# Optimization experiments

Hardware: AMD Instinct MI355X
Metric: run time of the kernel (lower is better)

Reference implementation:

```python
import jax, jax.numpy as jnp
import numpy as np

B, L, H = 4096, 4096, 1024  # batch, num_labels, hidden_size


def setup_inputs() -> dict:
    key = jax.random.key(0)
    k1, k2, k3, k4, k5 = jax.random.split(key, 5)
    return {
        "bert_output": jax.random.normal(k1, (B, H), dtype=jnp.float32),
        "label_embed": jax.random.normal(k2, (L, H), dtype=jnp.float32),
        "W": jax.random.normal(k3, (L, H), dtype=jnp.float32) * 0.02,
        "b": jax.random.normal(k4, (L,), dtype=jnp.float32) * 0.02,
        "labels": jax.random.randint(k5, (B, L), 0, 2, dtype=jnp.int32),
    }


def reference(bert_output, label_embed, W, b, labels):
    # Original: output[i, j] = classifier(bert_output[i] + label_embed[j])[j]
    #         = sum_k (x[i,k] + E[j,k]) * W[j,k] + b[j]
    #         = (x @ W^T)[i,j] + (E * W).sum(-1)[j] + b[j]
    xWt = jnp.einsum('bh,lh->bl', bert_output, W)          # [B, L] GEMM
    diag_bias = jnp.sum(label_embed * W, axis=-1) + b       # [L] epilogue
    logits = xWt + diag_bias[None, :]                       # [B, L]
    return logits
```

## Files before the change

### kernel.cpp

```cpp
#include <hip/hip_runtime.h>
#include <hip/hip_bf16.h>

#define Bdim 4096
#define Ldim 4096
#define Hdim 1024
#define BM 256
#define BN 256
#define BK 64
#define NT (Hdim / BK)

typedef __attribute__((ext_vector_type(8))) __bf16 bf16x8;
typedef __attribute__((ext_vector_type(4))) float floatx4;

__device__ __forceinline__ unsigned short f2bf(float f) {
  union { __hip_bfloat16 h; unsigned short u; } c;
  c.h = __float2bfloat16(f);
  return c.u;
}

__global__ __launch_bounds__(256) void prep_kernel(
    const float* __restrict__ X, const float* __restrict__ E,
    const float* __restrict__ W, const float* __restrict__ b,
    unsigned short* __restrict__ Xb, unsigned short* __restrict__ Wb,
    float* __restrict__ bias) {
  const int blk = blockIdx.x;
  const int t = threadIdx.x;
  if (blk < 1024) {
    const int wave = t >> 6;
    const int lane = t & 63;
    const int row = blk * 4 + wave;
    const float4* wrow = reinterpret_cast<const float4*>(W + (size_t)row * Hdim);
    const float4* erow = reinterpret_cast<const float4*>(E + (size_t)row * Hdim);
    ushort4* wbrow = reinterpret_cast<ushort4*>(Wb + (size_t)row * Hdim);
    float dot = 0.f;
#pragma unroll
    for (int j = 0; j < 4; ++j) {
      const int idx = lane + j * 64;
      const float4 wv = wrow[idx];
      const float4 ev = erow[idx];
      ushort4 o;
      o.x = f2bf(wv.x); o.y = f2bf(wv.y); o.z = f2bf(wv.z); o.w = f2bf(wv.w);
      wbrow[idx] = o;
      dot += wv.x * ev.x + wv.y * ev.y + wv.z * ev.z + wv.w * ev.w;
    }
#pragma unroll
    for (int off = 32; off > 0; off >>= 1) dot += __shfl_down(dot, off, 64);
    if (lane == 0) bias[row] = dot + b[row];
  } else {
    const int base = (blk - 1024) * 1024 + t;
    const float4* xs = reinterpret_cast<const float4*>(X);
    ushort4* xd = reinterpret_cast<ushort4*>(Xb);
#pragma unroll
    for (int j = 0; j < 4; ++j) {
      const float4 v = xs[base + j * 256];
      ushort4 o;
      o.x = f2bf(v.x); o.y = f2bf(v.y); o.z = f2bf(v.z); o.w = f2bf(v.w);
      xd[base + j * 256] = o;
    }
  }
}

__global__ __launch_bounds__(512, 2) void gemm_bias_kernel(
    const unsigned short* __restrict__ A,
    const unsigned short* __restrict__ Bw,
    const float* __restrict__ bias,
    float* __restrict__ C) {
  __shared__ __align__(16) unsigned short lds[2][2][BM * BK];

  const int tid = threadIdx.x;
  const int wave = tid >> 6;
  const int lane = tid & 63;
  const int wm = wave >> 2;
  const int wn = wave & 3;
  const int m_blk = blockIdx.y * BM;
  const int n_blk = blockIdx.x * BN;

  const int srow = wave * 8 + (lane >> 3);
  const int skofs = ((lane & 7) ^ (lane >> 3)) * 8;
  const unsigned short* gA = A + (size_t)(m_blk + srow) * Hdim + skofs;
  const unsigned short* gB = Bw + (size_t)(n_blk + srow) * Hdim + skofs;

  const int fr = lane & 15;
  const int fq = lane >> 4;
  const int kx0 = ((fq) ^ (fr & 7)) * 8;
  const int kx1 = ((4 + fq) ^ (fr & 7)) * 8;
  const int aBase = (wm * 128 + fr) * BK;
  const int bBase = (wn * 64 + fr) * BK;

  floatx4 acc[8][4] = {};
  bf16x8 af[8][2], bfv[4][2];

#define GLL(src, dst)                                                  \
  __builtin_amdgcn_global_load_lds(                                    \
      (const __attribute__((address_space(1))) void*)(src),            \
      (__attribute__((address_space(3))) void*)(dst), 16, 0, 0)

#define STAGE_H(c, mat, h, kt)                                         \
  do {                                                                 \
    const unsigned short* _g = (mat) ? gB : gA;                        \
    GLL(_g + (size_t)((h) * 128) * Hdim + (size_t)(kt) * BK,           \
        &lds[c][mat][((h) * 128 + wave * 8) * BK]);                    \
    GLL(_g + (size_t)((h) * 128 + 64) * Hdim + (size_t)(kt) * BK,      \
        &lds[c][mat][((h) * 128 + 64 + wave * 8) * BK]);               \
  } while (0)

#define READ_A(c, lo)                                                  \
  do {                                                                 \
    _Pragma("unroll") for (int mi = (lo); mi < (lo) + 4; ++mi) {       \
      af[mi][0] = *(const bf16x8*)&lds[c][0][aBase + mi * 16 * BK + kx0]; \
      af[mi][1] = *(const bf16x8*)&lds[c][0][aBase + mi * 16 * BK + kx1]; \
    }                                                                  \
  } while (0)

#define READ_B(c, lo)                                                  \
  do {                                                                 \
    _Pragma("unroll") for (int ni = (lo); ni < (lo) + 2; ++ni) {       \
      bfv[ni][0] = *(const bf16x8*)&lds[c][1][bBase + ni * 16 * BK + kx0]; \
      bfv[ni][1] = *(const bf16x8*)&lds[c][1][bBase + ni * 16 * BK + kx1]; \
    }                                                                  \
  } while (0)

#define MFMA_Q(M0, N0)                                                 \
  do {                                                                 \
    __builtin_amdgcn_s_setprio(1);                                     \
    _Pragma("unroll") for (int mi = (M0); mi < (M0) + 4; ++mi)         \
      _Pragma("unroll") for (int ni = (N0); ni < (N0) + 2; ++ni) {     \
        acc[mi][ni] = __builtin_amdgcn_mfma_f32_16x16x32_bf16(         \
            af[mi][0], bfv[ni][0], acc[mi][ni], 0, 0, 0);              \
        acc[mi][ni] = __builtin_amdgcn_mfma_f32_16x16x32_bf16(         \
            af[mi][1], bfv[ni][1], acc[mi][ni], 0, 0, 0);              \
      }                                                                \
    __builtin_amdgcn_s_setprio(0);                                     \
  } while (0)

#define BAR __builtin_amdgcn_s_barrier()
#define LGKM0 asm volatile("s_waitcnt lgkmcnt(0)" ::: "memory")
#define GATE4 asm volatile("s_waitcnt vmcnt(4)\n\ts_barrier" ::: "memory")
#define GATE0 asm volatile("s_waitcnt vmcnt(0)\n\ts_barrier" ::: "memory")

#define TILE_BODY(c, o, kt, DO_B, DO_A, GATE)                          \
  do {                                                                 \
                                                               \
    if (DO_B) STAGE_H(o, 1, 0, (kt) + 1);                              \
    READ_A(c, 0);                                                      \
    READ_B(c, 0);                                                      \
    BAR; LGKM0;                                                        \
    MFMA_Q(0, 0);                                                      \
                                                               \
    if (DO_B) STAGE_H(o, 1, 1, (kt) + 1);                              \
    READ_A(c, 4);                                                      \
    BAR; LGKM0;                                                        \
    MFMA_Q(4, 0);                                                      \
    BAR;   \
                                                               \
    if (DO_A) STAGE_H(c, 0, 0, (kt) + 2);                              \
    READ_B(c, 2);                                                      \
    BAR; LGKM0;                                                        \
    MFMA_Q(0, 2);                                                      \
    BAR;                  \
                                                               \
    if (DO_A) STAGE_H(c, 0, 1, (kt) + 2);                              \
    GATE;                                                              \
    MFMA_Q(4, 2);                                                      \
  } while (0)

  STAGE_H(0, 0, 0, 0);
  STAGE_H(0, 0, 1, 0);
  STAGE_H(0, 1, 0, 0);
  STAGE_H(0, 1, 1, 0);
  STAGE_H(1, 0, 0, 1);
  STAGE_H(1, 0, 1, 1);
  GATE4;

#pragma unroll 1
  for (int t = 0; t < NT - 2; t += 2) {
    TILE_BODY(0, 1, t, 1, 1, GATE4);
    TILE_BODY(1, 0, t + 1, 1, 1, GATE4);
  }
  TILE_BODY(0, 1, NT - 2, 1, 0, GATE0);
  TILE_BODY(1, 0, NT - 1, 0, 0, (void)0);

#undef GLL
#undef STAGE_H
#undef READ_A
#undef READ_B
#undef MFMA_Q
#undef BAR
#undef LGKM0
#undef GATE4
#undef GATE0
#undef TILE_BODY

  const int col0 = n_blk + wn * 64 + fr;
  const int row0 = m_blk + wm * 128 + fq * 4;
#pragma unroll
  for (int ni = 0; ni < 4; ++ni) {
    const float bs = bias[col0 + ni * 16];
#pragma unroll
    for (int mi = 0; mi < 8; ++mi) {
      float* cp = C + (size_t)(row0 + mi * 16) * Ldim + (col0 + ni * 16);
      floatx4 v = acc[mi][ni];
      cp[0 * (size_t)Ldim] = v.x + bs;
      cp[1 * (size_t)Ldim] = v.y + bs;
      cp[2 * (size_t)Ldim] = v.z + bs;
      cp[3 * (size_t)Ldim] = v.w + bs;
    }
  }
}

extern "C" void kernel_launch(void* const* d_in, const int* in_sizes, int n_in,
                              void* d_out, int out_size, void* d_ws, size_t ws_size,
                              hipStream_t stream) {
  const float* X = (const float*)d_in[0];
  const float* E = (const float*)d_in[1];
  const float* W = (const float*)d_in[2];
  const float* b = (const float*)d_in[3];
  float* out = (float*)d_out;

  unsigned short* Xb = (unsigned short*)d_ws;
  unsigned short* Wb = Xb + (size_t)Bdim * Hdim;
  float* bias = (float*)(Wb + (size_t)Ldim * Hdim);

  prep_kernel<<<2048, 256, 0, stream>>>(X, E, W, b, Xb, Wb, bias);
  dim3 grid(Ldim / BN, Bdim / BM);
  gemm_bias_kernel<<<grid, 512, 0, stream>>>(Xb, Wb, bias, out);
}
```

Measured before the change: 49.62 us.

## Shrink GEMM tile to 128x256x32 and raise occupancy to four blocks per CU

Halves the M tile and K step, cutting per-wave accumulators from 32 to 16 MFMA tiles. This lowers register and LDS use so launch bounds can request four blocks per SM instead of two. The staging and swizzle are rewritten for the 32-wide K slice, with a one-deep vmcnt gate, and the grid must double along M. The cost is lower arithmetic intensity per LDS byte and twice as many barrier-gated iterations, which raises global and LDS traffic per flop.

```diff
diff --git a/kernel.cpp b/kernel.cpp
--- a/kernel.cpp
+++ b/kernel.cpp
@@ -4,9 +4,9 @@
 #define Bdim 4096
 #define Ldim 4096
 #define Hdim 1024
-#define BM 256
+#define BM 128
 #define BN 256
-#define BK 64
+#define BK 32
 #define NT (Hdim / BK)
 
 typedef __attribute__((ext_vector_type(8))) __bf16 bf16x8;
@@ -60,12 +60,13 @@
   }
 }
 
-__global__ __launch_bounds__(512, 2) void gemm_bias_kernel(
+__global__ __launch_bounds__(512, 4) void gemm_bias_kernel(
     const unsigned short* __restrict__ A,
     const unsigned short* __restrict__ Bw,
     const float* __restrict__ bias,
     float* __restrict__ C) {
-  __shared__ __align__(16) unsigned short lds[2][2][BM * BK];
+  __shared__ __align__(16) unsigned short ldsA[2][BM * BK];
+  __shared__ __align__(16) unsigned short ldsB[2][BN * BK];
 
   const int tid = threadIdx.x;
   const int wave = tid >> 6;
@@ -75,129 +76,115 @@
   const int m_blk = blockIdx.y * BM;
   const int n_blk = blockIdx.x * BN;
 
-  const int srow = wave * 8 + (lane >> 3);
-  const int skofs = ((lane & 7) ^ (lane >> 3)) * 8;
+  const int srow = tid >> 2;
+  const int skofs = ((tid & 3) ^ ((tid >> 3) & 3)) * 8;
   const unsigned short* gA = A + (size_t)(m_blk + srow) * Hdim + skofs;
   const unsigned short* gB = Bw + (size_t)(n_blk + srow) * Hdim + skofs;
 
   const int fr = lane & 15;
   const int fq = lane >> 4;
-  const int kx0 = ((fq) ^ (fr & 7)) * 8;
-  const int kx1 = ((4 + fq) ^ (fr & 7)) * 8;
-  const int aBase = (wm * 128 + fr) * BK;
+  const int kx = (fq ^ ((fr >> 1) & 3)) * 8;
+  const int aBase = (wm * 64 + fr) * BK;
   const int bBase = (wn * 64 + fr) * BK;
 
-  floatx4 acc[8][4] = {};
-  bf16x8 af[8][2], bfv[4][2];
+  floatx4 acc[4][4] = {};
+  bf16x8 af[4], bfv[4];
 
 #define GLL(src, dst)                                                  \
   __builtin_amdgcn_global_load_lds(                                    \
       (const __attribute__((address_space(1))) void*)(src),            \
       (__attribute__((address_space(3))) void*)(dst), 16, 0, 0)
 
-#define STAGE_H(c, mat, h, kt)                                         \
-  do {                                                                 \
-    const unsigned short* _g = (mat) ? gB : gA;                        \
-    GLL(_g + (size_t)((h) * 128) * Hdim + (size_t)(kt) * BK,           \
-        &lds[c][mat][((h) * 128 + wave * 8) * BK]);                    \
-    GLL(_g + (size_t)((h) * 128 + 64) * Hdim + (size_t)(kt) * BK,      \
-        &lds[c][mat][((h) * 128 + 64 + wave * 8) * BK]);               \
-  } while (0)
+#define STAGE_A(c, kt) GLL(gA + (size_t)(kt) * BK, &ldsA[c][tid * 8])
+#define STAGE_B(c, h, kt)                                              \
+  GLL(gB + (size_t)((h) * 128) * Hdim + (size_t)(kt) * BK,             \
+      &ldsB[c][(h) * 128 * BK + tid * 8])
 
 #define READ_A(c, lo)                                                  \
   do {                                                                 \
-    _Pragma("unroll") for (int mi = (lo); mi < (lo) + 4; ++mi) {       \
-      af[mi][0] = *(const bf16x8*)&lds[c][0][aBase + mi * 16 * BK + kx0]; \
-      af[mi][1] = *(const bf16x8*)&lds[c][0][aBase + mi * 16 * BK + kx1]; \
-    }                                                                  \
+    _Pragma("unroll") for (int mi = (lo); mi < (lo) + 2; ++mi)         \
+      af[mi] = *(const bf16x8*)&ldsA[c][aBase + mi * 16 * BK + kx];    \
   } while (0)
 
 #define READ_B(c, lo)                                                  \
   do {                                                                 \
-    _Pragma("unroll") for (int ni = (lo); ni < (lo) + 2; ++ni) {       \
-      bfv[ni][0] = *(const bf16x8*)&lds[c][1][bBase + ni * 16 * BK + kx0]; \
-      bfv[ni][1] = *(const bf16x8*)&lds[c][1][bBase + ni * 16 * BK + kx1]; \
-    }                                                                  \
+    _Pragma("unroll") for (int ni = (lo); ni < (lo) + 2; ++ni)         \
+      bfv[ni] = *(const bf16x8*)&ldsB[c][bBase + ni * 16 * BK + kx];   \
   } while (0)
 
 #define MFMA_Q(M0, N0)                                                 \
   do {                                                                 \
     __builtin_amdgcn_s_setprio(1);                                     \
-    _Pragma("unroll") for (int mi = (M0); mi < (M0) + 4; ++mi)         \
-      _Pragma("unroll") for (int ni = (N0); ni < (N0) + 2; ++ni) {     \
+    _Pragma("unroll") for (int mi = (M0); mi < (M0) + 2; ++mi)         \
+      _Pragma("unroll") for (int ni = (N0); ni < (N0) + 2; ++ni)       \
         acc[mi][ni] = __builtin_amdgcn_mfma_f32_16x16x32_bf16(         \
-            af[mi][0], bfv[ni][0], acc[mi][ni], 0, 0, 0);              \
-        acc[mi][ni] = __builtin_amdgcn_mfma_f32_16x16x32_bf16(         \
-            af[mi][1], bfv[ni][1], acc[mi][ni], 0, 0, 0);              \
-      }                                                                \
+            af[mi], bfv[ni], acc[mi][ni], 0, 0, 0);                    \
     __builtin_amdgcn_s_setprio(0);                                     \
   } while (0)
 
 #define BAR __builtin_amdgcn_s_barrier()
 #define LGKM0 asm volatile("s_waitcnt lgkmcnt(0)" ::: "memory")
-#define GATE4 asm volatile("s_waitcnt vmcnt(4)\n\ts_barrier" ::: "memory")
+#define GATE1 asm volatile("s_waitcnt vmcnt(1)\n\ts_barrier" ::: "memory")
 #define GATE0 asm volatile("s_waitcnt vmcnt(0)\n\ts_barrier" ::: "memory")
 
 #define TILE_BODY(c, o, kt, DO_B, DO_A, GATE)                          \
   do {                                                                 \
                                                                \
-    if (DO_B) STAGE_H(o, 1, 0, (kt) + 1);                              \
+    if (DO_B) STAGE_B(o, 0, (kt) + 1);                                 \
     READ_A(c, 0);                                                      \
     READ_B(c, 0);                                                      \
     BAR; LGKM0;                                                        \
     MFMA_Q(0, 0);                                                      \
                                                                \
-    if (DO_B) STAGE_H(o, 1, 1, (kt) + 1);                              \
-    READ_A(c, 4);                                                      \
+    if (DO_B) STAGE_B(o, 1, (kt) + 1);                                 \
+    READ_A(c, 2);                                                      \
     BAR; LGKM0;                                                        \
-    MFMA_Q(4, 0);                                                      \
+    MFMA_Q(2, 0);                                                      \
     BAR;   \
                                                                \
-    if (DO_A) STAGE_H(c, 0, 0, (kt) + 2);                              \
+    if (DO_A) STAGE_A(c, (kt) + 2);                                    \
     READ_B(c, 2);                                                      \
     BAR; LGKM0;                                                        \
     MFMA_Q(0, 2);                                                      \
     BAR;                  \
                                                                \
-    if (DO_A) STAGE_H(c, 0, 1, (kt) + 2);                              \
     GATE;                                                              \
-    MFMA_Q(4, 2);                                                      \
-  } while (0)
-
-  STAGE_H(0, 0, 0, 0);
-  STAGE_H(0, 0, 1, 0);
-  STAGE_H(0, 1, 0, 0);
-  STAGE_H(0, 1, 1, 0);
-  STAGE_H(1, 0, 0, 1);
-  STAGE_H(1, 0, 1, 1);
-  GATE4;
+    MFMA_Q(2, 2);                                                      \
+  } while (0)
+
+  STAGE_A(0, 0);
+  STAGE_B(0, 0, 0);
+  STAGE_B(0, 1, 0);
+  STAGE_A(1, 1);
+  GATE1;
 
 #pragma unroll 1
   for (int t = 0; t < NT - 2; t += 2) {
-    TILE_BODY(0, 1, t, 1, 1, GATE4);
-    TILE_BODY(1, 0, t + 1, 1, 1, GATE4);
+    TILE_BODY(0, 1, t, 1, 1, GATE1);
+    TILE_BODY(1, 0, t + 1, 1, 1, GATE1);
   }
   TILE_BODY(0, 1, NT - 2, 1, 0, GATE0);
   TILE_BODY(1, 0, NT - 1, 0, 0, (void)0);
 
 #undef GLL
-#undef STAGE_H
+#undef STAGE_A
+#undef STAGE_B
 #undef READ_A
 #undef READ_B
 #undef MFMA_Q
 #undef BAR
 #undef LGKM0
-#undef GATE4
+#undef GATE1
 #undef GATE0
 #undef TILE_BODY
 
   const int col0 = n_blk + wn * 64 + fr;
-  const int row0 = m_blk + wm * 128 + fq * 4;
+  const int row0 = m_blk + wm * 64 + fq * 4;
 #pragma unroll
   for (int ni = 0; ni < 4; ++ni) {
     const float bs = bias[col0 + ni * 16];
 #pragma unroll
-    for (int mi = 0; mi < 8; ++mi) {
+    for (int mi = 0; mi < 4; ++mi) {
       float* cp = C + (size_t)(row0 + mi * 16) * Ldim + (col0 + ni * 16);
       floatx4 v = acc[mi][ni];
       cp[0 * (size_t)Ldim] = v.x + bs;
```

After: 58.04 us. +17.0%, slower.
